# Kernel tuning notes

Hardware: AMD Instinct MI355X
Metric: run time of the kernel (lower is better)

## Reference

```python
import jax, jax.numpy as jnp
import numpy as np

EMBED_DIM = 256
NUM_HEADS = 8
HEAD_DIM = EMBED_DIM // NUM_HEADS
LN_EPS = 1e-5


def _linear_init(key, fan_in, fan_out):
    # torch nn.Linear default: U(-1/sqrt(fan_in), 1/sqrt(fan_in)) for W and b
    kw, kb = jax.random.split(key)
    bound = 1.0 / np.sqrt(fan_in)
    W = jax.random.uniform(kw, (fan_out, fan_in), jnp.float32, -bound, bound)
    b = jax.random.uniform(kb, (fan_out,), jnp.float32, -bound, bound)
    return W, b


def setup_inputs() -> dict:
    key = jax.random.key(0)
    ks = jax.random.split(key, 6)
    x = jax.random.normal(ks[0], (2, 512, EMBED_DIM), jnp.float32)
    Wq, bq = _linear_init(ks[1], EMBED_DIM, EMBED_DIM)
    Wk, bk = _linear_init(ks[2], EMBED_DIM, EMBED_DIM)
    Wv, bv = _linear_init(ks[3], EMBED_DIM, EMBED_DIM)
    Wr, br = _linear_init(ks[4], EMBED_DIM, EMBED_DIM)
    Wo, bo = _linear_init(ks[5], EMBED_DIM, EMBED_DIM)
    g1 = jnp.ones((EMBED_DIM,), jnp.float32)
    b1 = jnp.zeros((EMBED_DIM,), jnp.float32)
    g2 = jnp.ones((EMBED_DIM,), jnp.float32)
    b2 = jnp.zeros((EMBED_DIM,), jnp.float32)
    return {"x": x, "Wq": Wq, "bq": bq, "Wk": Wk, "bk": bk, "Wv": Wv, "bv": bv,
            "Wr": Wr, "br": br, "Wo": Wo, "bo": bo,
            "g1": g1, "b1": b1, "g2": g2, "b2": b2}


def _layer_norm(x, g, b):
    mu = jnp.mean(x, axis=-1, keepdims=True)
    var = jnp.mean(jnp.square(x - mu), axis=-1, keepdims=True)
    return (x - mu) * jax.lax.rsqrt(var + LN_EPS) * g + b


def reference(x, Wq, bq, Wk, bk, Wv, bv, Wr, br, Wo, bo, g1, b1, g2, b2):
    B, N, D = x.shape
    H, Dh = NUM_HEADS, HEAD_DIM
    Q = x @ Wq.T + bq  # [B,N,D]
    K = x @ Wk.T + bk
    V = x @ Wv.T + bv
    # pairwise differences, projected: [B,N,N,D]
    R = x[:, :, None, :] - x[:, None, :, :]
    R = jnp.einsum('bijd,ed->bije', R, Wr) + br
    max_R1 = jnp.max(R, axis=1)  # [B,N,D] (max over rows -> bias for Q)
    max_R2 = jnp.max(R, axis=2)  # [B,N,D] (max over cols -> bias for K)
    Q_r = Q + max_R1
    K_r = K + max_R2
    # [B,H,N,Dh]
    Q_r = Q_r.reshape(B, N, H, Dh).transpose(0, 2, 1, 3)
    K_r = K_r.reshape(B, N, H, Dh).transpose(0, 2, 1, 3)
    Vh = V.reshape(B, N, H, Dh).transpose(0, 2, 1, 3)
    scores = jnp.einsum('bhqd,bhkd->bhqk', Q_r, K_r) / np.sqrt(Dh).astype(np.float32)
    probs = jax.nn.softmax(scores, axis=-1)
    attn = jnp.einsum('bhqk,bhkd->bhqd', probs, Vh)
    attn = attn.transpose(0, 2, 1, 3).reshape(B, N, D)
    attn = attn @ Wo.T + bo  # dropout is identity in eval mode
    h = _layer_norm(x + attn, g1, b1)
    return _layer_norm(h, g2, b2)
```

## Files before the change

### kernel.cpp

```cpp
#include <hip/hip_runtime.h>
#include <hip/hip_bf16.h>
#include <math.h>

#define NSEQ 512
#define EMB 256

typedef __attribute__((ext_vector_type(8))) short bf16x8;
typedef __attribute__((ext_vector_type(4))) float f32x4;

__device__ __forceinline__ unsigned short f2bf(float f) {
    unsigned u = __float_as_uint(f);
    unsigned r = (u + 0x7FFFu + ((u >> 16) & 1u)) >> 16;
    return (unsigned short)r;
}
__device__ __forceinline__ float bf2f(unsigned short s) {
    return __uint_as_float(((unsigned)s) << 16);
}
__device__ __forceinline__ ushort4 cvt4(float4 v) {
    ushort4 o;
    o.x = f2bf(v.x); o.y = f2bf(v.y); o.z = f2bf(v.z); o.w = f2bf(v.w);
    return o;
}

__global__ __launch_bounds__(256) void k_gemm_mfma(
    const float* __restrict__ X,
    const float* __restrict__ Wq, const float* __restrict__ Wk,
    const float* __restrict__ Wv, const float* __restrict__ Wr,
    const float* __restrict__ Wo,
    const float* __restrict__ bq, const float* __restrict__ bv,
    unsigned short* __restrict__ Qb, unsigned short* __restrict__ Kb,
    unsigned short* __restrict__ Vtb, unsigned short* __restrict__ Wob,
    float* __restrict__ maxPart)
{
    const int t = threadIdx.x;

    if (blockIdx.y == 16) {
        const float4* Wg = (const float4*)Wo;
        #pragma unroll
        for (int i = 0; i < 4; ++i) {
            int idx4 = blockIdx.x * 1024 + i * 256 + t;
            ((ushort4*)Wob)[idx4] = cvt4(Wg[idx4]);
        }
        return;
    }

    __shared__ __align__(16) unsigned short Xs[64 * 264];
    __shared__ __align__(16) unsigned short Ws[64 * 264];
    __shared__ float red[4][64];

    const int w = t >> 6, l = t & 63;
    const int ln = l & 15, kg = l >> 4;
    const int m0 = blockIdx.x * 64;
    const int nW = blockIdx.y * 64;
    const int seg = blockIdx.y >> 2;
    const int wbase = (blockIdx.y & 3) * 64;

    const float4* X4  = (const float4*)X;
    const float4* Wq4 = (const float4*)Wq;
    const float4* Wk4 = (const float4*)Wk;
    const float4* Wv4 = (const float4*)Wv;
    const float4* Wr4 = (const float4*)Wr;

    #pragma unroll
    for (int i = 0; i < 16; ++i) {
        int idx = i * 256 + t;
        int row = idx >> 6, c4 = idx & 63;
        float4 xv = X4[(size_t)(m0 + row) * 64 + c4];
        *(ushort4*)(Xs + row * 264 + c4 * 4) = cvt4(xv);

        size_t off = (size_t)(wbase + row) * 64 + c4;
        float4 wv;
        if (seg == 0) {
            float4 a = Wq4[off], r = Wr4[off];
            wv = make_float4(a.x - r.x, a.y - r.y, a.z - r.z, a.w - r.w);
        } else if (seg == 1) {
            float4 a = Wk4[off], r = Wr4[off];
            wv = make_float4(a.x + r.x, a.y + r.y, a.z + r.z, a.w + r.w);
        } else if (seg == 2) {
            wv = Wv4[off];
        } else {
            wv = Wr4[off];
        }
        *(ushort4*)(Ws + row * 264 + c4 * 4) = cvt4(wv);
    }
    __syncthreads();

    f32x4 acc[4] = {{0.f,0.f,0.f,0.f},{0.f,0.f,0.f,0.f},
                    {0.f,0.f,0.f,0.f},{0.f,0.f,0.f,0.f}};
    const int arow = (w << 4) + ln;
    #pragma unroll
    for (int ks = 0; ks < 8; ++ks) {
        bf16x8 a = *(const bf16x8*)(Xs + arow * 264 + ks * 32 + kg * 8);
        #pragma unroll
        for (int nf = 0; nf < 4; ++nf) {
            bf16x8 b = *(const bf16x8*)(Ws + (nf * 16 + ln) * 264 + ks * 32 + kg * 8);
            acc[nf] = __builtin_amdgcn_mfma_f32_16x16x32_bf16(a, b, acc[nf], 0, 0, 0);
        }
    }

    if (seg == 0) {
        #pragma unroll
        for (int nf = 0; nf < 4; ++nf) {
            int c = (nW & 255) + nf * 16 + ln;
            float bb = bq[c];
            #pragma unroll
            for (int r = 0; r < 4; ++r) {
                int row = m0 + w * 16 + kg * 4 + r;
                Qb[(size_t)row * 256 + c] = f2bf(acc[nf][r] + bb);
            }
        }
    } else if (seg == 1) {
        #pragma unroll
        for (int nf = 0; nf < 4; ++nf) {
            int c = (nW & 255) + nf * 16 + ln;
            #pragma unroll
            for (int r = 0; r < 4; ++r) {
                int row = m0 + w * 16 + kg * 4 + r;
                Kb[(size_t)row * 256 + c] = f2bf(acc[nf][r]);
            }
        }
    } else if (seg == 2) {
        #pragma unroll
        for (int nf = 0; nf < 4; ++nf) {
            int c = (nW & 255) + nf * 16 + ln;
            int h = c >> 5, d = c & 31;
            float bb = bv[c];
            #pragma unroll
            for (int r = 0; r < 4; ++r) {
                int row = m0 + w * 16 + kg * 4 + r;
                int b = row >> 9, ml = row & 511;
                Vtb[((size_t)(b * 8 + h) * 32 + d) * 512 + ml] = f2bf(acc[nf][r] + bb);
            }
        }
    } else {
        #pragma unroll
        for (int nf = 0; nf < 4; ++nf) {
            float mx = fmaxf(fmaxf(acc[nf][0], acc[nf][1]),
                             fmaxf(acc[nf][2], acc[nf][3]));
            mx = fmaxf(mx, __shfl_xor(mx, 16));
            mx = fmaxf(mx, __shfl_xor(mx, 32));
            if (l < 16) red[w][nf * 16 + ln] = mx;
        }
        __syncthreads();
        if (t < 64) {
            float m = fmaxf(fmaxf(red[0][t], red[1][t]),
                            fmaxf(red[2][t], red[3][t]));
            const int b = blockIdx.x >> 3;
            const int mblk = blockIdx.x & 7;
            maxPart[b * 2048 + mblk * 256 + (nW & 255) + t] = m;
        }
    }
}

__global__ __launch_bounds__(256) void k_attn_og(
    const unsigned short* __restrict__ Qb,
    const unsigned short* __restrict__ Kb,
    const unsigned short* __restrict__ Vtb,
    const unsigned short* __restrict__ Wob,
    const float* __restrict__ maxPart,
    const float* __restrict__ br,
    unsigned short* __restrict__ yPh)
{
    __shared__ __align__(16) unsigned short Plds[4][32][136];
    __shared__ float Olds[4][32][33];
    __shared__ float mlds[4][32], llds[4][32];
    __shared__ float scl[4][32], Li[32];
    __shared__ float qadd[32];
    __shared__ __align__(16) unsigned short Ob[32][36];

    const int t = threadIdx.x;
    const int w = t >> 6, l = t & 63;
    const int ln = l & 15, kg = l >> 4;
    const int q0 = blockIdx.x * 32;
    const int h = blockIdx.y, bz = blockIdx.z;
    const int e0 = h * 32;
    const int bh = bz * 8 + h;
    const float scale = 0.17677669529663687f;

    if (t < 32) {
        float m = maxPart[bz * 2048 + e0 + t];
        #pragma unroll
        for (int j = 1; j < 8; ++j)
            m = fmaxf(m, maxPart[bz * 2048 + j * 256 + e0 + t]);
        qadd[t] = m + br[e0 + t];
    }
    __syncthreads();

    bf16x8 af[2];
    #pragma unroll
    for (int qf = 0; qf < 2; ++qf) {
        size_t qrow = (size_t)(bz * NSEQ + q0 + qf * 16 + ln) * 256 + e0 + kg * 8;
        bf16x8 qa = *(const bf16x8*)(Qb + qrow);
        #pragma unroll
        for (int j = 0; j < 8; ++j) {
            int d = kg * 8 + j;
            af[qf][j] = (short)f2bf((bf2f((unsigned short)qa[j]) + qadd[d]) * scale);
        }
    }

    const int key0 = w * 128;
    f32x4 sc[2][8];
    #pragma unroll
    for (int kf = 0; kf < 8; ++kf) {
        size_t krow = (size_t)(bz * NSEQ + key0 + kf * 16 + ln) * 256 + e0 + kg * 8;
        bf16x8 bfr = *(const bf16x8*)(Kb + krow);
        f32x4 z = {0.f, 0.f, 0.f, 0.f};
        sc[0][kf] = __builtin_amdgcn_mfma_f32_16x16x32_bf16(af[0], bfr, z, 0, 0, 0);
        sc[1][kf] = __builtin_amdgcn_mfma_f32_16x16x32_bf16(af[1], bfr, z, 0, 0, 0);
    }

    float m_[2][4], l_[2][4];
    #pragma unroll
    for (int qf = 0; qf < 2; ++qf) {
        #pragma unroll
        for (int r = 0; r < 4; ++r) {
            float mx = sc[qf][0][r];
            #pragma unroll
            for (int kf = 1; kf < 8; ++kf) mx = fmaxf(mx, sc[qf][kf][r]);
            #pragma unroll
            for (int off = 1; off < 16; off <<= 1) mx = fmaxf(mx, __shfl_xor(mx, off));
            m_[qf][r] = mx;
            float s = 0.f;
            #pragma unroll
            for (int kf = 0; kf < 8; ++kf) {
                float p = __expf(sc[qf][kf][r] - mx);
                sc[qf][kf][r] = p;
                s += p;
            }
            #pragma unroll
            for (int off = 1; off < 16; off <<= 1) s += __shfl_xor(s, off);
            l_[qf][r] = s;
        }
    }

    #pragma unroll
    for (int qf = 0; qf < 2; ++qf)
        #pragma unroll
        for (int kf = 0; kf < 8; ++kf)
            #pragma unroll
            for (int r = 0; r < 4; ++r)
                Plds[w][qf * 16 + kg * 4 + r][kf * 16 + ln] = f2bf(sc[qf][kf][r]);

    f32x4 o[2][2] = {{{0.f,0.f,0.f,0.f},{0.f,0.f,0.f,0.f}},
                     {{0.f,0.f,0.f,0.f},{0.f,0.f,0.f,0.f}}};
    #pragma unroll
    for (int ks = 0; ks < 4; ++ks) {
        bf16x8 vf[2];
        #pragma unroll
        for (int df = 0; df < 2; ++df) {
            size_t vrow = ((size_t)bh * 32 + df * 16 + ln) * 512 + key0 + ks * 32 + kg * 8;
            vf[df] = *(const bf16x8*)(Vtb + vrow);
        }
        #pragma unroll
        for (int qf = 0; qf < 2; ++qf) {
            bf16x8 pf = *(const bf16x8*)&Plds[w][qf * 16 + ln][ks * 32 + kg * 8];
            o[qf][0] = __builtin_amdgcn_mfma_f32_16x16x32_bf16(pf, vf[0], o[qf][0], 0, 0, 0);
            o[qf][1] = __builtin_amdgcn_mfma_f32_16x16x32_bf16(pf, vf[1], o[qf][1], 0, 0, 0);
        }
    }

    if (ln == 0) {
        #pragma unroll
        for (int qf = 0; qf < 2; ++qf)
            #pragma unroll
            for (int r = 0; r < 4; ++r) {
                mlds[w][qf * 16 + kg * 4 + r] = m_[qf][r];
                llds[w][qf * 16 + kg * 4 + r] = l_[qf][r];
            }
    }
    #pragma unroll
    for (int qf = 0; qf < 2; ++qf)
        #pragma unroll
        for (int df = 0; df < 2; ++df)
            #pragma unroll
            for (int r = 0; r < 4; ++r)
                Olds[w][qf * 16 + kg * 4 + r][df * 16 + ln] = o[qf][df][r];
    __syncthreads();

    if (t < 32) {
        float M = fmaxf(fmaxf(mlds[0][t], mlds[1][t]),
                        fmaxf(mlds[2][t], mlds[3][t]));
        float L = 0.f;
        #pragma unroll
        for (int wv = 0; wv < 4; ++wv) {
            float s = __expf(mlds[wv][t] - M);
            scl[wv][t] = s;
            L += s * llds[wv][t];
        }
        Li[t] = 1.f / L;
    }
    __syncthreads();

    #pragma unroll
    for (int i = 0; i < 4; ++i) {
        int idx = t + 256 * i;
        int q = idx >> 5, d = idx & 31;
        float acc = 0.f;
        #pragma unroll
        for (int wv = 0; wv < 4; ++wv)
            acc += scl[wv][q] * Olds[wv][q][d];
        Ob[q][d] = f2bf(acc * Li[q]);
    }
    __syncthreads();

    bf16x8 aog[2];
    #pragma unroll
    for (int qf = 0; qf < 2; ++qf)
        aog[qf] = *(const bf16x8*)&Ob[qf * 16 + ln][kg * 8];

    unsigned short* dst = yPh + (size_t)h * (1024 * 256);
    #pragma unroll
    for (int nf = 0; nf < 4; ++nf) {
        int n = w * 64 + nf * 16 + ln;
        bf16x8 bfr = *(const bf16x8*)(Wob + (size_t)n * 256 + e0 + kg * 8);
        f32x4 z = {0.f, 0.f, 0.f, 0.f};
        f32x4 y0 = __builtin_amdgcn_mfma_f32_16x16x32_bf16(aog[0], bfr, z, 0, 0, 0);
        f32x4 y1 = __builtin_amdgcn_mfma_f32_16x16x32_bf16(aog[1], bfr, z, 0, 0, 0);
        #pragma unroll
        for (int r = 0; r < 4; ++r) {
            size_t row0 = (size_t)(bz * NSEQ + q0 + kg * 4 + r);
            dst[row0 * 256 + n] = f2bf(y0[r]);
            dst[(row0 + 16) * 256 + n] = f2bf(y1[r]);
        }
    }
}

__global__ __launch_bounds__(256) void k_lnorm(
    const unsigned short* __restrict__ yPh, const float* __restrict__ x,
    const float* __restrict__ bo,
    const float* __restrict__ g1, const float* __restrict__ b1,
    const float* __restrict__ g2, const float* __restrict__ b2,
    float* __restrict__ out)
{
    __shared__ float red[4][4][2];
    const int t = threadIdx.x;
    const int r0 = blockIdx.x * 4;
    const int c = t;
    const int wid = t >> 6, lane = t & 63;

    float y[4];
    #pragma unroll
    for (int r = 0; r < 4; ++r) {
        size_t off = (size_t)(r0 + r) * 256 + c;
        float acc = x[off] + bo[c];
        #pragma unroll
        for (int h = 0; h < 8; ++h)
            acc += bf2f(yPh[(size_t)h * 262144 + off]);
        y[r] = acc;
    }

    #pragma unroll
    for (int r = 0; r < 4; ++r) {
        float s = y[r], s2 = y[r] * y[r];
        #pragma unroll
        for (int off = 32; off > 0; off >>= 1) {
            s  += __shfl_xor(s, off);
            s2 += __shfl_xor(s2, off);
        }
        if (lane == 0) { red[wid][r][0] = s; red[wid][r][1] = s2; }
    }
    __syncthreads();
    float t1[4];
    #pragma unroll
    for (int r = 0; r < 4; ++r) {
        float s  = red[0][r][0] + red[1][r][0] + red[2][r][0] + red[3][r][0];
        float s2 = red[0][r][1] + red[1][r][1] + red[2][r][1] + red[3][r][1];
        float mu = s * (1.f / 256.f);
        float var = s2 * (1.f / 256.f) - mu * mu;
        float rs = rsqrtf(var + 1e-5f);
        t1[r] = (y[r] - mu) * rs * g1[c] + b1[c];
    }
    __syncthreads();

    #pragma unroll
    for (int r = 0; r < 4; ++r) {
        float s = t1[r], s2 = t1[r] * t1[r];
        #pragma unroll
        for (int off = 32; off > 0; off >>= 1) {
            s  += __shfl_xor(s, off);
            s2 += __shfl_xor(s2, off);
        }
        if (lane == 0) { red[wid][r][0] = s; red[wid][r][1] = s2; }
    }
    __syncthreads();
    #pragma unroll
    for (int r = 0; r < 4; ++r) {
        float s  = red[0][r][0] + red[1][r][0] + red[2][r][0] + red[3][r][0];
        float s2 = red[0][r][1] + red[1][r][1] + red[2][r][1] + red[3][r][1];
        float mu = s * (1.f / 256.f);
        float var = s2 * (1.f / 256.f) - mu * mu;
        float rs = rsqrtf(var + 1e-5f);
        out[(size_t)(r0 + r) * 256 + c] = (t1[r] - mu) * rs * g2[c] + b2[c];
    }
}

extern "C" void kernel_launch(void* const* d_in, const int* in_sizes, int n_in,
                              void* d_out, int out_size, void* d_ws, size_t ws_size,
                              hipStream_t stream)
{
    const float* x  = (const float*)d_in[0];
    const float* Wq = (const float*)d_in[1];
    const float* bq = (const float*)d_in[2];
    const float* Wk = (const float*)d_in[3];
    const float* bk = (const float*)d_in[4];
    const float* Wv = (const float*)d_in[5];
    const float* bv = (const float*)d_in[6];
    const float* Wr = (const float*)d_in[7];
    const float* br = (const float*)d_in[8];
    const float* Wo = (const float*)d_in[9];
    const float* bo = (const float*)d_in[10];
    const float* g1 = (const float*)d_in[11];
    const float* b1 = (const float*)d_in[12];
    const float* g2 = (const float*)d_in[13];
    const float* b2 = (const float*)d_in[14];
    float* out = (float*)d_out;
    (void)bk;

    unsigned short* u = (unsigned short*)d_ws;
    unsigned short* Qb   = u;
    unsigned short* Kb   = u + 262144;
    unsigned short* Vtb  = u + 524288;
    unsigned short* Wob  = u + 786432;
    float* maxPart = (float*)(u + 851968);
    unsigned short* yPh = u + 860160;

    k_gemm_mfma<<<dim3(16, 17), 256, 0, stream>>>(x, Wq, Wk, Wv, Wr, Wo, bq, bv,
                                                  Qb, Kb, Vtb, Wob, maxPart);
    k_attn_og<<<dim3(16, 8, 2), 256, 0, stream>>>(Qb, Kb, Vtb, Wob, maxPart,
                                                  br, yPh);
    k_lnorm<<<256, 256, 0, stream>>>(yPh, x, bo, g1, b1, g2, b2, out);
}
```

Before: 27.28 us.

## Fuse layernorm into attention via last-block atomic counter; load X fragments directly

Removes the separate layernorm kernel. Each attention block bumps a per-(batch, query-tile) atomic counter after writing its per-head partial output, and the last of the 8 head blocks sums the partials and applies both layernorms for those 32 rows. The counter is reset inside the GEMM kernel. Separately, the GEMM now loads X rows straight from global memory into registers as bf16 MFMA fragments instead of staging them through LDS. This saves one kernel launch and some LDS traffic, but the final layernorm work is serialized onto 32 tail blocks and X reads become less coalesced.

```diff
diff --git a/kernel.cpp b/kernel.cpp
--- a/kernel.cpp
+++ b/kernel.cpp
@@ -30,11 +30,13 @@
     const float* __restrict__ bq, const float* __restrict__ bv,
     unsigned short* __restrict__ Qb, unsigned short* __restrict__ Kb,
     unsigned short* __restrict__ Vtb, unsigned short* __restrict__ Wob,
-    float* __restrict__ maxPart)
+    float* __restrict__ maxPart,
+    unsigned* __restrict__ cnt)
 {
     const int t = threadIdx.x;
 
     if (blockIdx.y == 16) {
+        if (blockIdx.x == 0 && t < 32) cnt[t] = 0u;
         const float4* Wg = (const float4*)Wo;
         #pragma unroll
         for (int i = 0; i < 4; ++i) {
@@ -44,7 +46,6 @@
         return;
     }
 
-    __shared__ __align__(16) unsigned short Xs[64 * 264];
     __shared__ __align__(16) unsigned short Ws[64 * 264];
     __shared__ float red[4][64];
 
@@ -55,19 +56,28 @@
     const int seg = blockIdx.y >> 2;
     const int wbase = (blockIdx.y & 3) * 64;
 
-    const float4* X4  = (const float4*)X;
+    const int arow = (w << 4) + ln;
+    const float* Xrow = X + (size_t)(m0 + arow) * 256 + kg * 8;
+    bf16x8 af[8];
+    #pragma unroll
+    for (int ks = 0; ks < 8; ++ks) {
+        float4 a0 = *(const float4*)(Xrow + ks * 32);
+        float4 a1 = *(const float4*)(Xrow + ks * 32 + 4);
+        ushort4 c0 = cvt4(a0), c1 = cvt4(a1);
+        af[ks][0] = (short)c0.x; af[ks][1] = (short)c0.y;
+        af[ks][2] = (short)c0.z; af[ks][3] = (short)c0.w;
+        af[ks][4] = (short)c1.x; af[ks][5] = (short)c1.y;
+        af[ks][6] = (short)c1.z; af[ks][7] = (short)c1.w;
+    }
+
     const float4* Wq4 = (const float4*)Wq;
     const float4* Wk4 = (const float4*)Wk;
     const float4* Wv4 = (const float4*)Wv;
     const float4* Wr4 = (const float4*)Wr;
-
     #pragma unroll
     for (int i = 0; i < 16; ++i) {
         int idx = i * 256 + t;
         int row = idx >> 6, c4 = idx & 63;
-        float4 xv = X4[(size_t)(m0 + row) * 64 + c4];
-        *(ushort4*)(Xs + row * 264 + c4 * 4) = cvt4(xv);
-
         size_t off = (size_t)(wbase + row) * 64 + c4;
         float4 wv;
         if (seg == 0) {
@@ -87,14 +97,12 @@
 
     f32x4 acc[4] = {{0.f,0.f,0.f,0.f},{0.f,0.f,0.f,0.f},
                     {0.f,0.f,0.f,0.f},{0.f,0.f,0.f,0.f}};
-    const int arow = (w << 4) + ln;
     #pragma unroll
     for (int ks = 0; ks < 8; ++ks) {
-        bf16x8 a = *(const bf16x8*)(Xs + arow * 264 + ks * 32 + kg * 8);
         #pragma unroll
         for (int nf = 0; nf < 4; ++nf) {
             bf16x8 b = *(const bf16x8*)(Ws + (nf * 16 + ln) * 264 + ks * 32 + kg * 8);
-            acc[nf] = __builtin_amdgcn_mfma_f32_16x16x32_bf16(a, b, acc[nf], 0, 0, 0);
+            acc[nf] = __builtin_amdgcn_mfma_f32_16x16x32_bf16(af[ks], b, acc[nf], 0, 0, 0);
         }
     }
 
@@ -159,7 +167,12 @@
     const unsigned short* __restrict__ Wob,
     const float* __restrict__ maxPart,
     const float* __restrict__ br,
-    unsigned short* __restrict__ yPh)
+    const float* __restrict__ x, const float* __restrict__ bo,
+    const float* __restrict__ g1, const float* __restrict__ b1,
+    const float* __restrict__ g2, const float* __restrict__ b2,
+    unsigned short* __restrict__ yPh,
+    unsigned* __restrict__ cnt,
+    float* __restrict__ out)
 {
     __shared__ __align__(16) unsigned short Plds[4][32][136];
     __shared__ float Olds[4][32][33];
@@ -167,6 +180,8 @@
     __shared__ float scl[4][32], Li[32];
     __shared__ float qadd[32];
     __shared__ __align__(16) unsigned short Ob[32][36];
+    __shared__ float lnred[4][4][2];
+    __shared__ unsigned doneOld;
 
     const int t = threadIdx.x;
     const int w = t >> 6, l = t & 63;
@@ -323,74 +338,70 @@
             dst[(row0 + 16) * 256 + n] = f2bf(y1[r]);
         }
     }
-}
-
-__global__ __launch_bounds__(256) void k_lnorm(
-    const unsigned short* __restrict__ yPh, const float* __restrict__ x,
-    const float* __restrict__ bo,
-    const float* __restrict__ g1, const float* __restrict__ b1,
-    const float* __restrict__ g2, const float* __restrict__ b2,
-    float* __restrict__ out)
-{
-    __shared__ float red[4][4][2];
-    const int t = threadIdx.x;
-    const int r0 = blockIdx.x * 4;
+
+    __threadfence();
+    if (t == 0) doneOld = atomicAdd(&cnt[bz * 16 + blockIdx.x], 1u);
+    __syncthreads();
+    if (doneOld != 7u) return;
+    __threadfence();
+
     const int c = t;
     const int wid = t >> 6, lane = t & 63;
-
-    float y[4];
-    #pragma unroll
-    for (int r = 0; r < 4; ++r) {
-        size_t off = (size_t)(r0 + r) * 256 + c;
-        float acc = x[off] + bo[c];
-        #pragma unroll
-        for (int h = 0; h < 8; ++h)
-            acc += bf2f(yPh[(size_t)h * 262144 + off]);
-        y[r] = acc;
-    }
-
-    #pragma unroll
-    for (int r = 0; r < 4; ++r) {
-        float s = y[r], s2 = y[r] * y[r];
-        #pragma unroll
-        for (int off = 32; off > 0; off >>= 1) {
-            s  += __shfl_xor(s, off);
-            s2 += __shfl_xor(s2, off);
-        }
-        if (lane == 0) { red[wid][r][0] = s; red[wid][r][1] = s2; }
-    }
-    __syncthreads();
-    float t1[4];
-    #pragma unroll
-    for (int r = 0; r < 4; ++r) {
-        float s  = red[0][r][0] + red[1][r][0] + red[2][r][0] + red[3][r][0];
-        float s2 = red[0][r][1] + red[1][r][1] + red[2][r][1] + red[3][r][1];
-        float mu = s * (1.f / 256.f);
-        float var = s2 * (1.f / 256.f) - mu * mu;
-        float rs = rsqrtf(var + 1e-5f);
-        t1[r] = (y[r] - mu) * rs * g1[c] + b1[c];
-    }
-    __syncthreads();
-
-    #pragma unroll
-    for (int r = 0; r < 4; ++r) {
-        float s = t1[r], s2 = t1[r] * t1[r];
-        #pragma unroll
-        for (int off = 32; off > 0; off >>= 1) {
-            s  += __shfl_xor(s, off);
-            s2 += __shfl_xor(s2, off);
-        }
-        if (lane == 0) { red[wid][r][0] = s; red[wid][r][1] = s2; }
-    }
-    __syncthreads();
-    #pragma unroll
-    for (int r = 0; r < 4; ++r) {
-        float s  = red[0][r][0] + red[1][r][0] + red[2][r][0] + red[3][r][0];
-        float s2 = red[0][r][1] + red[1][r][1] + red[2][r][1] + red[3][r][1];
-        float mu = s * (1.f / 256.f);
-        float var = s2 * (1.f / 256.f) - mu * mu;
-        float rs = rsqrtf(var + 1e-5f);
-        out[(size_t)(r0 + r) * 256 + c] = (t1[r] - mu) * rs * g2[c] + b2[c];
+    for (int rg = 0; rg < 8; ++rg) {
+        const size_t r0 = (size_t)(bz * NSEQ + q0 + rg * 4);
+        float y[4];
+        #pragma unroll
+        for (int r = 0; r < 4; ++r) {
+            size_t off = (r0 + r) * 256 + c;
+            float acc = x[off] + bo[c];
+            #pragma unroll
+            for (int hh = 0; hh < 8; ++hh)
+                acc += bf2f(yPh[(size_t)hh * 262144 + off]);
+            y[r] = acc;
+        }
+        __syncthreads();
+        #pragma unroll
+        for (int r = 0; r < 4; ++r) {
+            float s = y[r], s2 = y[r] * y[r];
+            #pragma unroll
+            for (int off = 32; off > 0; off >>= 1) {
+                s  += __shfl_xor(s, off);
+                s2 += __shfl_xor(s2, off);
+            }
+            if (lane == 0) { lnred[wid][r][0] = s; lnred[wid][r][1] = s2; }
+        }
+        __syncthreads();
+        float t1[4];
+        #pragma unroll
+        for (int r = 0; r < 4; ++r) {
+            float s  = lnred[0][r][0] + lnred[1][r][0] + lnred[2][r][0] + lnred[3][r][0];
+            float s2 = lnred[0][r][1] + lnred[1][r][1] + lnred[2][r][1] + lnred[3][r][1];
+            float mu = s * (1.f / 256.f);
+            float var = s2 * (1.f / 256.f) - mu * mu;
+            float rs = rsqrtf(var + 1e-5f);
+            t1[r] = (y[r] - mu) * rs * g1[c] + b1[c];
+        }
+        __syncthreads();
+        #pragma unroll
+        for (int r = 0; r < 4; ++r) {
+            float s = t1[r], s2 = t1[r] * t1[r];
+            #pragma unroll
+            for (int off = 32; off > 0; off >>= 1) {
+                s  += __shfl_xor(s, off);
+                s2 += __shfl_xor(s2, off);
+            }
+            if (lane == 0) { lnred[wid][r][0] = s; lnred[wid][r][1] = s2; }
+        }
+        __syncthreads();
+        #pragma unroll
+        for (int r = 0; r < 4; ++r) {
+            float s  = lnred[0][r][0] + lnred[1][r][0] + lnred[2][r][0] + lnred[3][r][0];
+            float s2 = lnred[0][r][1] + lnred[1][r][1] + lnred[2][r][1] + lnred[3][r][1];
+            float mu = s * (1.f / 256.f);
+            float var = s2 * (1.f / 256.f) - mu * mu;
+            float rs = rsqrtf(var + 1e-5f);
+            out[(r0 + r) * 256 + c] = (t1[r] - mu) * rs * g2[c] + b2[c];
+        }
     }
 }
 
@@ -422,11 +433,12 @@
     unsigned short* Vtb  = u + 524288;
     unsigned short* Wob  = u + 786432;
     float* maxPart = (float*)(u + 851968);
-    unsigned short* yPh = u + 860160;
+    unsigned* cnt  = (unsigned*)(u + 860160);
+    unsigned short* yPh = u + 860224;
 
     k_gemm_mfma<<<dim3(16, 17), 256, 0, stream>>>(x, Wq, Wk, Wv, Wr, Wo, bq, bv,
-                                                  Qb, Kb, Vtb, Wob, maxPart);
-    k_attn_og<<<dim3(16, 8, 2), 256, 0, stream>>>(Qb, Kb, Vtb, Wob, maxPart,
-                                                  br, yPh);
-    k_lnorm<<<256, 256, 0, stream>>>(yPh, x, bo, g1, b1, g2, b2, out);
-}
+                                                  Qb, Kb, Vtb, Wob, maxPart, cnt);
+    k_attn_og<<<dim3(16, 8, 2), 256, 0, stream>>>(Qb, Kb, Vtb, Wob, maxPart, br,
+                                                  x, bo, g1, b1, g2, b2,
+                                                  yPh, cnt, out);
+}
```

Result: slower. 77.92 us (+185.7%).
